# Kernel tuning notes

Hardware: AMD Instinct MI355X
Metric: run time of the kernel (lower is better)

Reference implementation:

```python
import jax, jax.numpy as jnp
import numpy as np

B, A, NC = 2_000_000, 3, 3  # batch, anchors per sample, num classes


def setup_inputs() -> dict:
    key = jax.random.key(0)
    k1, k2, k3, k4 = jax.random.split(key, 4)
    # output: probabilities in (0,1) since BCELoss expects probs (sigmoid already applied upstream)
    output = jax.random.uniform(k1, (B, A, 1 + 3 + NC), dtype=jnp.float32,
                                minval=1e-4, maxval=1.0 - 1e-4)
    # target: [obj in {0,1} | 3 coords | class index as float]
    obj = jax.random.bernoulli(k2, 0.5, (B, A)).astype(jnp.float32)
    coords = jax.random.uniform(k3, (B, A, 3), dtype=jnp.float32)
    cls = jax.random.randint(k4, (B, A), 0, NC).astype(jnp.float32)
    target = jnp.concatenate([obj[..., None], coords, cls[..., None]], axis=-1)
    return {"output": output, "target": target}


def _bce_sum(p, t):
    # matches torch.nn.BCELoss(reduction='sum'), which clamps log terms at -100
    logp = jnp.maximum(jnp.log(p), -100.0)
    log1mp = jnp.maximum(jnp.log1p(-p), -100.0)
    return -jnp.sum(t * logp + (1.0 - t) * log1mp)


def reference(output, target):
    obj_col = target[:, :, 0]
    target_object = (obj_col == 1.0).astype(output.dtype)
    # one-hot class target (vectorized replacement of the Python scatter loop)
    cls_idx = jax.lax.stop_gradient(target[:, :, -1]).astype(jnp.int32)
    target_classe = jax.nn.one_hot(cls_idx, NC, dtype=output.dtype)  # [B, A, NC]

    xywh_loss = jnp.sum((output[:, :, 1:4] - target[:, :, 1:4]) ** 2)
    class_loss = _bce_sum(output[:, :, 4:], target_classe)
    object_loss = _bce_sum(output[:, :, 0], target_object)
    # note: the original also computes noObjectLoss but never uses it
    return 2.0 * class_loss + 4.0 * xywh_loss + object_loss
```

## Files before the change

kernel.cpp:

```cpp
#include <hip/hip_runtime.h>


#define NROWS   6000000
#define NQUANTA (NROWS / 64)
#define GRID    2048
#define BLOCK   256
#define NWAVES  (GRID * (BLOCK / 64))
#define LN2     0.69314718055994530942

#define GLOAD_LDS(g, l) __builtin_amdgcn_global_load_lds(                     \
    (const __attribute__((address_space(1))) unsigned int*)(g),               \
    (__attribute__((address_space(3))) unsigned int*)(l), 4, 0, 0)

__global__ __launch_bounds__(256) void det_loss_kernel(
        const float* __restrict__ out,
        const float* __restrict__ tgt,
        double* __restrict__ partial) {
    __shared__ float lds_out[4][448];
    __shared__ float lds_tgt[4][320];

    const int lane  = threadIdx.x & 63;
    const int wid   = threadIdx.x >> 6;
    const int gwave = blockIdx.x * 4 + wid;

    float* lo = lds_out[wid];
    float* lt = lds_tgt[wid];

    float xywh_sum = 0.0f;
    float log2_sum = 0.0f;

    for (int q = gwave; q < NQUANTA; q += NWAVES) {
        asm volatile("s_waitcnt lgkmcnt(0)" ::: "memory");
        const float* po = out + (size_t)q * 448 + lane;
        const float* pt = tgt + (size_t)q * 320 + lane;
        #pragma unroll
        for (int k = 0; k < 7; ++k)
            GLOAD_LDS(po + k * 64, lo + k * 64);
        #pragma unroll
        for (int k = 0; k < 5; ++k)
            GLOAD_LDS(pt + k * 64, lt + k * 64);
        asm volatile("s_waitcnt vmcnt(0)" ::: "memory");

        const int b7 = lane * 7;
        const int b5 = lane * 5;
        float o0 = lo[b7 + 0], o1 = lo[b7 + 1], o2 = lo[b7 + 2], o3 = lo[b7 + 3];
        float o4 = lo[b7 + 4], o5 = lo[b7 + 5], o6 = lo[b7 + 6];
        float t0 = lt[b5 + 0], t1 = lt[b5 + 1], t2 = lt[b5 + 2], t3 = lt[b5 + 3];
        float t4 = lt[b5 + 4];

        float dx = o1 - t1, dy = o2 - t2, dz = o3 - t3;
        xywh_sum += dx * dx + dy * dy + dz * dz;

        int ci = (int)t4;
        float f0 = (ci == 0) ? o4 : 1.0f - o4;
        float f1 = (ci == 1) ? o5 : 1.0f - o5;
        float f2 = (ci == 2) ? o6 : 1.0f - o6;
        float fo = (t0 == 1.0f) ? o0 : 1.0f - o0;
        float m  = f0 * f1 * f2;
        float v  = m * m * fo;
        log2_sum += __log2f(v);
    }

    double val = 4.0 * (double)xywh_sum - LN2 * (double)log2_sum;
    #pragma unroll
    for (int off = 32; off > 0; off >>= 1)
        val += __shfl_down(val, off, 64);

    __shared__ double wsum[4];
    if (lane == 0) wsum[wid] = val;
    __syncthreads();
    if (threadIdx.x == 0)
        partial[blockIdx.x] = wsum[0] + wsum[1] + wsum[2] + wsum[3];
}

__global__ __launch_bounds__(256) void final_reduce(
        const double* __restrict__ partial, float* __restrict__ outp) {
    double s = 0.0;
    for (int i = threadIdx.x; i < GRID; i += BLOCK) s += partial[i];
    #pragma unroll
    for (int off = 32; off > 0; off >>= 1)
        s += __shfl_down(s, off, 64);
    __shared__ double wsum[4];
    const int lane = threadIdx.x & 63;
    const int wid  = threadIdx.x >> 6;
    if (lane == 0) wsum[wid] = s;
    __syncthreads();
    if (threadIdx.x == 0)
        outp[0] = (float)(wsum[0] + wsum[1] + wsum[2] + wsum[3]);
}

extern "C" void kernel_launch(void* const* d_in, const int* in_sizes, int n_in,
                              void* d_out, int out_size, void* d_ws, size_t ws_size,
                              hipStream_t stream) {
    const float* out_p = (const float*)d_in[0];
    const float* tgt_p = (const float*)d_in[1];
    float* res = (float*)d_out;
    double* ws = (double*)d_ws;

    det_loss_kernel<<<GRID, BLOCK, 0, stream>>>(out_p, tgt_p, ws);
    final_reduce<<<1, BLOCK, 0, stream>>>(ws, res);
}
```

Baseline: 309.0 us.

## Double-buffer 16-byte global-to-LDS loads with one-wave blocks and larger quanta

Replaces the per-wave synchronous 4-byte global_load_lds loop with single-wave blocks that prefetch 256-row tiles into two LDS buffers using 16-byte direct loads. The next tile is in flight while the current one is read out with float4 LDS reads and reduced. This hides memory latency behind compute and cuts load instruction count. The cost is more LDS per block, a hand-tuned vmcnt wait scheme and a separate scalar tail path handled by block 0.

```diff
diff --git a/kernel.cpp b/kernel.cpp
--- a/kernel.cpp
+++ b/kernel.cpp
@@ -1,82 +1,131 @@
 #include <hip/hip_runtime.h>
 
 
-#define NROWS   6000000
-#define NQUANTA (NROWS / 64)
-#define GRID    2048
-#define BLOCK   256
-#define NWAVES  (GRID * (BLOCK / 64))
-#define LN2     0.69314718055994530942
+#define NROWS     6000000
+#define QROWS     256
+#define NQ        (NROWS / QROWS)
+#define TAILSTART (NQ * QROWS)
+#define GRID      1536
+#define BLOCK     64
+#define LN2       0.69314718055994530942
 
-#define GLOAD_LDS(g, l) __builtin_amdgcn_global_load_lds(                     \
+#define GL16(g, l) __builtin_amdgcn_global_load_lds(                          \
     (const __attribute__((address_space(1))) unsigned int*)(g),               \
-    (__attribute__((address_space(3))) unsigned int*)(l), 4, 0, 0)
+    (__attribute__((address_space(3))) unsigned int*)(l), 16, 0, 0)
 
-__global__ __launch_bounds__(256) void det_loss_kernel(
-        const float* __restrict__ out,
-        const float* __restrict__ tgt,
+__device__ __forceinline__ float row_terms(
+        const float* o, const float* t, float* xywh) {
+    float dx = o[1] - t[1], dy = o[2] - t[2], dz = o[3] - t[3];
+    *xywh += dx * dx + dy * dy + dz * dz;
+    int ci = (int)t[4];
+    float f0 = (ci == 0) ? o[4] : 1.0f - o[4];
+    float f1 = (ci == 1) ? o[5] : 1.0f - o[5];
+    float f2 = (ci == 2) ? o[6] : 1.0f - o[6];
+    float fo = (t[0] == 1.0f) ? o[0] : 1.0f - o[0];
+    float m = f0 * f1 * f2;
+    return __log2f(m * m * fo);
+}
+
+__global__ __launch_bounds__(64) void det_loss_kernel(
+        const float* __restrict__ outp,
+        const float* __restrict__ tgtp,
         double* __restrict__ partial) {
-    __shared__ float lds_out[4][448];
-    __shared__ float lds_tgt[4][320];
+    __shared__ float lds[2][3072];
+    const int lane = threadIdx.x;
+    const int w = blockIdx.x;
 
-    const int lane  = threadIdx.x & 63;
-    const int wid   = threadIdx.x >> 6;
-    const int gwave = blockIdx.x * 4 + wid;
+    const int nmine = (NQ - 1 - w) / GRID + 1;
 
-    float* lo = lds_out[wid];
-    float* lt = lds_tgt[wid];
-
-    float xywh_sum = 0.0f;
-    float log2_sum = 0.0f;
-
-    for (int q = gwave; q < NQUANTA; q += NWAVES) {
-        asm volatile("s_waitcnt lgkmcnt(0)" ::: "memory");
-        const float* po = out + (size_t)q * 448 + lane;
-        const float* pt = tgt + (size_t)q * 320 + lane;
+    {
+        const float* so = outp + (size_t)w * (QROWS * 7);
+        const float* st = tgtp + (size_t)w * (QROWS * 5);
+        float* dst = &lds[0][0];
         #pragma unroll
-        for (int k = 0; k < 7; ++k)
-            GLOAD_LDS(po + k * 64, lo + k * 64);
+        for (int c = 0; c < 7; ++c) GL16(so + c * 256 + lane * 4, dst + c * 256);
         #pragma unroll
-        for (int k = 0; k < 5; ++k)
-            GLOAD_LDS(pt + k * 64, lt + k * 64);
-        asm volatile("s_waitcnt vmcnt(0)" ::: "memory");
-
-        const int b7 = lane * 7;
-        const int b5 = lane * 5;
-        float o0 = lo[b7 + 0], o1 = lo[b7 + 1], o2 = lo[b7 + 2], o3 = lo[b7 + 3];
-        float o4 = lo[b7 + 4], o5 = lo[b7 + 5], o6 = lo[b7 + 6];
-        float t0 = lt[b5 + 0], t1 = lt[b5 + 1], t2 = lt[b5 + 2], t3 = lt[b5 + 3];
-        float t4 = lt[b5 + 4];
-
-        float dx = o1 - t1, dy = o2 - t2, dz = o3 - t3;
-        xywh_sum += dx * dx + dy * dy + dz * dz;
-
-        int ci = (int)t4;
-        float f0 = (ci == 0) ? o4 : 1.0f - o4;
-        float f1 = (ci == 1) ? o5 : 1.0f - o5;
-        float f2 = (ci == 2) ? o6 : 1.0f - o6;
-        float fo = (t0 == 1.0f) ? o0 : 1.0f - o0;
-        float m  = f0 * f1 * f2;
-        float v  = m * m * fo;
-        log2_sum += __log2f(v);
+        for (int c = 0; c < 5; ++c) GL16(st + c * 256 + lane * 4, dst + 1792 + c * 256);
+    }
+    if (nmine > 1) {
+        const size_t q = (size_t)w + GRID;
+        const float* so = outp + q * (QROWS * 7);
+        const float* st = tgtp + q * (QROWS * 5);
+        float* dst = &lds[1][0];
+        #pragma unroll
+        for (int c = 0; c < 7; ++c) GL16(so + c * 256 + lane * 4, dst + c * 256);
+        #pragma unroll
+        for (int c = 0; c < 5; ++c) GL16(st + c * 256 + lane * 4, dst + 1792 + c * 256);
     }
 
-    double val = 4.0 * (double)xywh_sum - LN2 * (double)log2_sum;
+    double acc = 0.0;
+    int cur = 0;
+    for (int t = 0; t < nmine; ++t) {
+        if (t + 1 < nmine) { asm volatile("s_waitcnt vmcnt(12)" ::: "memory"); }
+        else               { asm volatile("s_waitcnt vmcnt(0)"  ::: "memory"); }
+
+        float of[28], tf[20];
+        {
+            const float* bo = &lds[cur][0] + lane * 28;
+            #pragma unroll
+            for (int k = 0; k < 7; ++k) {
+                float4 v = *reinterpret_cast<const float4*>(bo + 4 * k);
+                of[4*k+0] = v.x; of[4*k+1] = v.y; of[4*k+2] = v.z; of[4*k+3] = v.w;
+            }
+            const float* bt = &lds[cur][1792] + lane * 20;
+            #pragma unroll
+            for (int k = 0; k < 5; ++k) {
+                float4 v = *reinterpret_cast<const float4*>(bt + 4 * k);
+                tf[4*k+0] = v.x; tf[4*k+1] = v.y; tf[4*k+2] = v.z; tf[4*k+3] = v.w;
+            }
+        }
+        asm volatile("s_waitcnt lgkmcnt(0)" ::: "memory");
+        __builtin_amdgcn_sched_barrier(0);
+
+        if (t + 2 < nmine) {
+            const size_t q = (size_t)w + (size_t)(t + 2) * GRID;
+            const float* so = outp + q * (QROWS * 7);
+            const float* st = tgtp + q * (QROWS * 5);
+            float* dst = &lds[cur][0];
+            #pragma unroll
+            for (int c = 0; c < 7; ++c) GL16(so + c * 256 + lane * 4, dst + c * 256);
+            #pragma unroll
+            for (int c = 0; c < 5; ++c) GL16(st + c * 256 + lane * 4, dst + 1792 + c * 256);
+        }
+
+        float xy = 0.0f, lg = 0.0f;
+        #pragma unroll
+        for (int r = 0; r < 4; ++r)
+            lg += row_terms(of + 7 * r, tf + 5 * r, &xy);
+        acc += 4.0 * (double)xy - LN2 * (double)lg;
+        cur ^= 1;
+    }
+
+    if (w == 0) {
+        int r = TAILSTART + lane * 2;
+        #pragma unroll
+        for (int rr = 0; rr < 2; ++rr) {
+            const float* o = outp + (size_t)(r + rr) * 7;
+            const float* t = tgtp + (size_t)(r + rr) * 5;
+            float ob[7], tb[5];
+            #pragma unroll
+            for (int j = 0; j < 7; ++j) ob[j] = o[j];
+            #pragma unroll
+            for (int j = 0; j < 5; ++j) tb[j] = t[j];
+            float xy = 0.0f;
+            float lg = row_terms(ob, tb, &xy);
+            acc += 4.0 * (double)xy - LN2 * (double)lg;
+        }
+    }
+
     #pragma unroll
     for (int off = 32; off > 0; off >>= 1)
-        val += __shfl_down(val, off, 64);
-
-    __shared__ double wsum[4];
-    if (lane == 0) wsum[wid] = val;
-    __syncthreads();
-    if (threadIdx.x == 0)
-        partial[blockIdx.x] = wsum[0] + wsum[1] + wsum[2] + wsum[3];
+        acc += __shfl_down(acc, off, 64);
+    if (lane == 0) partial[w] = acc;
 }
 
 __global__ __launch_bounds__(256) void final_reduce(
         const double* __restrict__ partial, float* __restrict__ outp) {
     double s = 0.0;
-    for (int i = threadIdx.x; i < GRID; i += BLOCK) s += partial[i];
+    for (int i = threadIdx.x; i < GRID; i += 256) s += partial[i];
     #pragma unroll
     for (int off = 32; off > 0; off >>= 1)
         s += __shfl_down(s, off, 64);
@@ -98,5 +147,5 @@
     double* ws = (double*)d_ws;
 
     det_loss_kernel<<<GRID, BLOCK, 0, stream>>>(out_p, tgt_p, ws);
-    final_reduce<<<1, BLOCK, 0, stream>>>(ws, res);
+    final_reduce<<<1, 256, 0, stream>>>(ws, res);
 }
```

Result: no change. 306.6 us (-0.8%).
